# Optimization experiments

Hardware: AMD Instinct MI355X
Metric: run time of the kernel (lower is better)

## Reference

```python
import jax, jax.numpy as jnp
from jax import lax
import numpy as np

F = 257  # frequency bins; input feature dim is 2*F (mag | probability)
EPS = 1e-07


def setup_inputs() -> dict:
    key = jax.random.key(0)
    B, T = 64, 2000
    # mag (positive) and probability (in [0,1]) both drawn uniform [0,1)
    inputs = jax.random.uniform(key, (B, T, 2 * F), dtype=jnp.float32)
    # parameters, initialized as in Garch_cell.build (constants)
    Alpha = jnp.full((F,), 0.5, dtype=jnp.float32)
    beta = jnp.full((F,), 1.0, dtype=jnp.float32)
    gamma = jnp.full((F,), 0.3, dtype=jnp.float32)
    eta = jnp.full((F,), 0.6, dtype=jnp.float32)
    pi = jnp.full((F,), 1.0, dtype=jnp.float32)
    return {"inputs": inputs, "Alpha": Alpha, "beta": beta, "gamma": gamma,
            "eta": eta, "pi": pi}


def reference(inputs, Alpha, beta, gamma, eta, pi):
    # inputs: [B, T, 2F]
    mag0 = inputs[:, 0, :F]
    prob0 = inputs[:, 0, F:]
    s_init = jnp.square(mag0 * (1.0 - prob0))  # [B, F]
    carry0 = (s_init, s_init)  # (nosiy_square, ceta_e)

    x_t = jnp.swapaxes(inputs, 0, 1)  # [T, B, 2F]

    def step(carry, xt):
        s0, s1 = carry
        mag = xt[:, :F]
        p = xt[:, F:]
        mag_sq = mag * mag
        nosiy_sq = (Alpha * s0 + (1.0 - Alpha) * mag_sq) * (1.0 - p) \
                   + (beta + gamma * s1 + eta * s0) * p
        # elu(alpha=0) == relu
        clean = jax.nn.relu(mag - jnp.sqrt(nosiy_sq + EPS))
        ceta_e = jax.nn.relu(mag_sq - pi * clean * clean)
        return (nosiy_sq, ceta_e), clean

    _, outs = lax.scan(step, carry0, x_t)  # outs: [T, B, F]
    return jnp.swapaxes(outs, 0, 1)  # [B, T, F]
```

## Files before the change

### kernel.cpp

```cpp
#include <hip/hip_runtime.h>
#include <cstdint>


#define GB 64
#define GT 2000
#define GF 257
#define GEPS 1e-7f

constexpr int S2f   = 2 * GF;
constexpr int ROWB  = S2f * 4;
constexpr int OROWB = GF * 4;
constexpr int NCH   = GT / 2;
constexpr int RB    = 24;
constexpr int UNROLL = 24;

typedef float v4f  __attribute__((ext_vector_type(4)));
typedef float v4fu __attribute__((ext_vector_type(4), aligned(4)));

#define STEP(mg, pp, cv)                                                  \
  {                                                                       \
    float msq_ = (mg) * (mg);                                             \
    float u_   = fmaf(am1, msq_, a * s0);                                 \
    float v_   = fmaf(e, s0, fmaf(g, s1, be));                            \
    float ns_  = fmaf(u_, 1.0f - (pp), v_ * (pp));                        \
    float cc_  = (mg) - __builtin_amdgcn_sqrtf(ns_ + GEPS);               \
    cc_ = fmaxf(cc_, 0.0f);                                               \
    s1 = fmaxf(fmaf(-pw, cc_ * cc_, msq_), 0.0f);                         \
    s0 = ns_;                                                             \
    (cv) = cc_;                                                           \
  }

__global__ __launch_bounds__(64) void garch_kernel(
    const float* __restrict__ in,
    const float* __restrict__ Alpha,
    const float* __restrict__ beta,
    const float* __restrict__ gamma,
    const float* __restrict__ eta,
    const float* __restrict__ pi,
    float* __restrict__ out)
{
  __shared__ v4f lring[4][64];
  __shared__ __align__(16) float ob[512];
  __shared__ float td[2 * GT];

  const int lane = threadIdx.x;
  const int blk  = blockIdx.x;

  if (blk < 256) {
    const int b  = blk >> 2;
    const int f0 = (blk & 3) << 6;
    const int f  = f0 + lane;

    const float a   = Alpha[f];
    const float be  = beta[f];
    const float g   = gamma[f];
    const float e   = eta[f];
    const float pw  = pi[f];
    const float am1 = 1.0f - a;

    const uint8_t* gb = (const uint8_t*)in + (size_t)b * GT * ROWB;
    const int sub = lane >> 4;
    const int q   = lane & 15;
    const uint8_t* gsrc = gb + (size_t)(sub >> 1) * ROWB
                             + (size_t)(sub & 1) * (GF * 4)
                             + (size_t)f0 * 4 + (size_t)q * 16;

    const float* lc0 = (const float*)&lring[0][0];

    uint8_t* stp = (uint8_t*)out + (size_t)b * GT * OROWB
                 + (size_t)(lane >> 4) * OROWB
                 + (size_t)f0 * 4 + (size_t)q * 16;

    v4fu rb[RB];
    #pragma unroll
    for (int c = 2; c <= 24; ++c)
      rb[c % RB] = *(const v4fu*)(gsrc + (size_t)c * (2 * ROWB));
    {
      v4fu t0 = *(const v4fu*)(gsrc);
      v4fu t1 = *(const v4fu*)(gsrc + (size_t)(2 * ROWB));
      lring[0][lane] = t0;
      lring[1][lane] = t1;
    }

    float s0 = 0.0f, s1 = 0.0f;

    for (int sbi = 0; sbi < 1008; sbi += UNROLL) {
      #pragma unroll
      for (int u = 0; u < UNROLL; ++u) {
        const int s = sbi + u;
        if (s + 25 < NCH)
          rb[(u + 1) % RB] =
              *(const v4fu*)(gsrc + (size_t)(s + 25) * (2 * ROWB));
        __builtin_amdgcn_sched_barrier(0);
        if (s < NCH) {
          const float* lc = lc0 + (size_t)(u & 3) * 256;
          const float mg0 = lc[lane];
          const float p0  = lc[64 + lane];
          const float mg1 = lc[128 + lane];
          const float p1  = lc[192 + lane];
          if (s == 0) {
            float t = mg0 * (1.0f - p0);
            s0 = s1 = t * t;
          }
          float c0, c1;
          STEP(mg0, p0, c0);
          STEP(mg1, p1, c1);
          const int h = (u >> 1) & 1;
          ob[h * 256 + (u & 1) * 128 + lane]      = c0;
          ob[h * 256 + (u & 1) * 128 + 64 + lane] = c1;
          if ((u & 1) && s >= 3) {
            v4f od = ((const v4f*)ob)[(1 - h) * 64 + lane];
            *(v4fu*)stp = od;
            stp += 4 * OROWB;
          }
        }
        if (s + 2 < NCH)
          lring[(u + 2) & 3][lane] = rb[(u + 2) % RB];
      }
    }
    {
      v4f od = ((const v4f*)ob)[64 + lane];
      *(v4fu*)stp = od;
    }
  } else {
    const int b = blk - 256;
    const float a   = Alpha[GF - 1];
    const float be  = beta[GF - 1];
    const float g   = gamma[GF - 1];
    const float e   = eta[GF - 1];
    const float pw  = pi[GF - 1];
    const float am1 = 1.0f - a;

    const float* prow = in + (size_t)b * GT * S2f;

    float mreg[32], preg[32];
    #pragma unroll
    for (int k = 0; k < 32; ++k) {
      const int t = lane + (k << 6);
      if (t < GT) {
        mreg[k] = prow[(size_t)t * S2f + (GF - 1)];
        preg[k] = prow[(size_t)t * S2f + (2 * GF - 1)];
      }
    }
    #pragma unroll
    for (int k = 0; k < 32; ++k) {
      const int t = lane + (k << 6);
      if (t < GT) {
        td[2 * t]     = mreg[k];
        td[2 * t + 1] = preg[k];
      }
    }
    __syncthreads();

    float m0 = td[0], p0 = td[1];
    float tt = m0 * (1.0f - p0);
    float s0 = tt * tt, s1 = s0;

    for (int j = 0; j < GT / 16; ++j) {
      float mv[16], pv[16];
      #pragma unroll
      for (int r = 0; r < 16; ++r) {
        mv[r] = td[2 * (16 * j + r)];
        pv[r] = td[2 * (16 * j + r) + 1];
      }
      float creg = 0.0f;
      #pragma unroll
      for (int r = 0; r < 16; ++r) {
        float cc;
        STEP(mv[r], pv[r], cc);
        if (lane == r) creg = cc;
      }
      if (lane < 16)
        out[((size_t)(b * GT + 16 * j + lane)) * GF + (GF - 1)] = creg;
    }
  }
}

extern "C" void kernel_launch(void* const* d_in, const int* in_sizes, int n_in,
                              void* d_out, int out_size, void* d_ws, size_t ws_size,
                              hipStream_t stream) {
  const float* in    = (const float*)d_in[0];
  const float* Alpha = (const float*)d_in[1];
  const float* beta  = (const float*)d_in[2];
  const float* gamma = (const float*)d_in[3];
  const float* eta   = (const float*)d_in[4];
  const float* pi    = (const float*)d_in[5];
  float* out = (float*)d_out;

  garch_kernel<<<320, 64, 0, stream>>>(in, Alpha, beta, gamma, eta, pi, out);
}
```

Measured before the change: 482.6 us.

## Add helper wavefront that prefetches input rows into cache ahead of compute

Each block grows to two wavefronts. The second wavefront issues throwaway global loads up to a fixed number of chunks ahead of the compute wavefront, throttled by a workgroup-shared progress counter, so the compute wave's own loads hit in cache. The recurrence is latency-bound, and this targets its global-load stalls. In exchange it adds spin-polling with sleeps, extra memory traffic, and an extra wave per block competing for issue slots.

```diff
diff --git a/kernel.cpp b/kernel.cpp
--- a/kernel.cpp
+++ b/kernel.cpp
@@ -13,6 +13,7 @@
 constexpr int NCH   = GT / 2;
 constexpr int RB    = 24;
 constexpr int UNROLL = 24;
+constexpr int AHEAD = 48;
 
 typedef float v4f  __attribute__((ext_vector_type(4)));
 typedef float v4fu __attribute__((ext_vector_type(4), aligned(4)));
@@ -25,12 +26,12 @@
     float ns_  = fmaf(u_, 1.0f - (pp), v_ * (pp));                        \
     float cc_  = (mg) - __builtin_amdgcn_sqrtf(ns_ + GEPS);               \
     cc_ = fmaxf(cc_, 0.0f);                                               \
-    s1 = fmaxf(fmaf(-pw, cc_ * cc_, msq_), 0.0f);                         \
+    s1 = fmaxf(fmaf(-pw, cc_ * cc_, msq_), 0.0f);                        \
     s0 = ns_;                                                             \
     (cv) = cc_;                                                           \
   }
 
-__global__ __launch_bounds__(64) void garch_kernel(
+__global__ __launch_bounds__(128) void garch_kernel(
     const float* __restrict__ in,
     const float* __restrict__ Alpha,
     const float* __restrict__ beta,
@@ -42,21 +43,16 @@
   __shared__ v4f lring[4][64];
   __shared__ __align__(16) float ob[512];
   __shared__ float td[2 * GT];
-
-  const int lane = threadIdx.x;
+  __shared__ uint32_t prog;
+
+  const int tid  = threadIdx.x;
+  const int w    = tid >> 6;
+  const int lane = tid & 63;
   const int blk  = blockIdx.x;
 
   if (blk < 256) {
     const int b  = blk >> 2;
     const int f0 = (blk & 3) << 6;
-    const int f  = f0 + lane;
-
-    const float a   = Alpha[f];
-    const float be  = beta[f];
-    const float g   = gamma[f];
-    const float e   = eta[f];
-    const float pw  = pi[f];
-    const float am1 = 1.0f - a;
 
     const uint8_t* gb = (const uint8_t*)in + (size_t)b * GT * ROWB;
     const int sub = lane >> 4;
@@ -65,86 +61,109 @@
                              + (size_t)(sub & 1) * (GF * 4)
                              + (size_t)f0 * 4 + (size_t)q * 16;
 
-    const float* lc0 = (const float*)&lring[0][0];
-
-    uint8_t* stp = (uint8_t*)out + (size_t)b * GT * OROWB
-                 + (size_t)(lane >> 4) * OROWB
-                 + (size_t)f0 * 4 + (size_t)q * 16;
-
-    v4fu rb[RB];
-    #pragma unroll
-    for (int c = 2; c <= 24; ++c)
-      rb[c % RB] = *(const v4fu*)(gsrc + (size_t)c * (2 * ROWB));
-    {
-      v4fu t0 = *(const v4fu*)(gsrc);
-      v4fu t1 = *(const v4fu*)(gsrc + (size_t)(2 * ROWB));
-      lring[0][lane] = t0;
-      lring[1][lane] = t1;
-    }
-
-    float s0 = 0.0f, s1 = 0.0f;
-
-    for (int sbi = 0; sbi < 1008; sbi += UNROLL) {
+    if (tid == 0) prog = 0;
+    __syncthreads();
+
+    if (w == 0) {
+      const int f = f0 + lane;
+      const float a   = Alpha[f];
+      const float be  = beta[f];
+      const float g   = gamma[f];
+      const float e   = eta[f];
+      const float pw  = pi[f];
+      const float am1 = 1.0f - a;
+
+      const float* lc0 = (const float*)&lring[0][0];
+
+      uint8_t* stp = (uint8_t*)out + (size_t)b * GT * OROWB
+                   + (size_t)(lane >> 4) * OROWB
+                   + (size_t)f0 * 4 + (size_t)q * 16;
+
+      v4fu rb[RB];
       #pragma unroll
-      for (int u = 0; u < UNROLL; ++u) {
-        const int s = sbi + u;
-        if (s + 25 < NCH)
-          rb[(u + 1) % RB] =
-              *(const v4fu*)(gsrc + (size_t)(s + 25) * (2 * ROWB));
-        __builtin_amdgcn_sched_barrier(0);
-        if (s < NCH) {
-          const float* lc = lc0 + (size_t)(u & 3) * 256;
-          const float mg0 = lc[lane];
-          const float p0  = lc[64 + lane];
-          const float mg1 = lc[128 + lane];
-          const float p1  = lc[192 + lane];
-          if (s == 0) {
-            float t = mg0 * (1.0f - p0);
-            s0 = s1 = t * t;
+      for (int c = 2; c <= 24; ++c)
+        rb[c % RB] = *(const v4fu*)(gsrc + (size_t)c * (2 * ROWB));
+      {
+        v4fu t0 = *(const v4fu*)(gsrc);
+        v4fu t1 = *(const v4fu*)(gsrc + (size_t)(2 * ROWB));
+        lring[0][lane] = t0;
+        lring[1][lane] = t1;
+      }
+
+      float s0 = 0.0f, s1 = 0.0f;
+
+      for (int sbi = 0; sbi < 1008; sbi += UNROLL) {
+        #pragma unroll
+        for (int u = 0; u < UNROLL; ++u) {
+          const int s = sbi + u;
+          if (s + 25 < NCH)
+            rb[(u + 1) % RB] =
+                *(const v4fu*)(gsrc + (size_t)(s + 25) * (2 * ROWB));
+          __builtin_amdgcn_sched_barrier(0);
+          if (s < NCH) {
+            if ((u & 7) == 0 && lane == 0)
+              __hip_atomic_store(&prog, (uint32_t)s, __ATOMIC_RELAXED,
+                                 __HIP_MEMORY_SCOPE_WORKGROUP);
+            const float* lc = lc0 + (size_t)(u & 3) * 256;
+            const float mg0 = lc[lane];
+            const float p0  = lc[64 + lane];
+            const float mg1 = lc[128 + lane];
+            const float p1  = lc[192 + lane];
+            if (s == 0) {
+              float t = mg0 * (1.0f - p0);
+              s0 = s1 = t * t;
+            }
+            float c0, c1;
+            STEP(mg0, p0, c0);
+            STEP(mg1, p1, c1);
+            const int h = (u >> 1) & 1;
+            ob[h * 256 + (u & 1) * 128 + lane]      = c0;
+            ob[h * 256 + (u & 1) * 128 + 64 + lane] = c1;
+            if ((u & 1) && s >= 3) {
+              v4f od = ((const v4f*)ob)[(1 - h) * 64 + lane];
+              *(v4fu*)stp = od;
+              stp += 4 * OROWB;
+            }
           }
-          float c0, c1;
-          STEP(mg0, p0, c0);
-          STEP(mg1, p1, c1);
-          const int h = (u >> 1) & 1;
-          ob[h * 256 + (u & 1) * 128 + lane]      = c0;
-          ob[h * 256 + (u & 1) * 128 + 64 + lane] = c1;
-          if ((u & 1) && s >= 3) {
-            v4f od = ((const v4f*)ob)[(1 - h) * 64 + lane];
-            *(v4fu*)stp = od;
-            stp += 4 * OROWB;
-          }
-        }
-        if (s + 2 < NCH)
-          lring[(u + 2) & 3][lane] = rb[(u + 2) % RB];
-      }
-    }
-    {
-      v4f od = ((const v4f*)ob)[64 + lane];
-      *(v4fu*)stp = od;
+          if (s + 2 < NCH)
+            lring[(u + 2) & 3][lane] = rb[(u + 2) % RB];
+        }
+      }
+      {
+        v4f od = ((const v4f*)ob)[64 + lane];
+        *(v4fu*)stp = od;
+      }
+    } else {
+      for (int c = 24; c < NCH; ++c) {
+        while (true) {
+          uint32_t pr = __hip_atomic_load(&prog, __ATOMIC_RELAXED,
+                                          __HIP_MEMORY_SCOPE_WORKGROUP);
+          if (c - (int)pr <= AHEAD) break;
+          __builtin_amdgcn_s_sleep(2);
+        }
+        v4f dummy;
+        asm volatile("global_load_dwordx4 %0, %1, off"
+                     : "=v"(dummy)
+                     : "v"((uint64_t)(uintptr_t)(gsrc +
+                            (size_t)c * (2 * ROWB))));
+      }
     }
   } else {
     const int b = blk - 256;
-    const float a   = Alpha[GF - 1];
-    const float be  = beta[GF - 1];
-    const float g   = gamma[GF - 1];
-    const float e   = eta[GF - 1];
-    const float pw  = pi[GF - 1];
-    const float am1 = 1.0f - a;
-
     const float* prow = in + (size_t)b * GT * S2f;
 
-    float mreg[32], preg[32];
+    float mreg[16], preg[16];
     #pragma unroll
-    for (int k = 0; k < 32; ++k) {
-      const int t = lane + (k << 6);
+    for (int k = 0; k < 16; ++k) {
+      const int t = tid + (k << 7);
       if (t < GT) {
         mreg[k] = prow[(size_t)t * S2f + (GF - 1)];
         preg[k] = prow[(size_t)t * S2f + (2 * GF - 1)];
       }
     }
     #pragma unroll
-    for (int k = 0; k < 32; ++k) {
-      const int t = lane + (k << 6);
+    for (int k = 0; k < 16; ++k) {
+      const int t = tid + (k << 7);
       if (t < GT) {
         td[2 * t]     = mreg[k];
         td[2 * t + 1] = preg[k];
@@ -152,26 +171,35 @@
     }
     __syncthreads();
 
-    float m0 = td[0], p0 = td[1];
-    float tt = m0 * (1.0f - p0);
-    float s0 = tt * tt, s1 = s0;
-
-    for (int j = 0; j < GT / 16; ++j) {
-      float mv[16], pv[16];
-      #pragma unroll
-      for (int r = 0; r < 16; ++r) {
-        mv[r] = td[2 * (16 * j + r)];
-        pv[r] = td[2 * (16 * j + r) + 1];
-      }
-      float creg = 0.0f;
-      #pragma unroll
-      for (int r = 0; r < 16; ++r) {
-        float cc;
-        STEP(mv[r], pv[r], cc);
-        if (lane == r) creg = cc;
-      }
-      if (lane < 16)
-        out[((size_t)(b * GT + 16 * j + lane)) * GF + (GF - 1)] = creg;
+    if (tid < 64) {
+      const float a   = Alpha[GF - 1];
+      const float be  = beta[GF - 1];
+      const float g   = gamma[GF - 1];
+      const float e   = eta[GF - 1];
+      const float pw  = pi[GF - 1];
+      const float am1 = 1.0f - a;
+
+      float m0 = td[0], p0 = td[1];
+      float tt = m0 * (1.0f - p0);
+      float s0 = tt * tt, s1 = s0;
+
+      for (int j = 0; j < GT / 16; ++j) {
+        float mv[16], pv[16];
+        #pragma unroll
+        for (int r = 0; r < 16; ++r) {
+          mv[r] = td[2 * (16 * j + r)];
+          pv[r] = td[2 * (16 * j + r) + 1];
+        }
+        float creg = 0.0f;
+        #pragma unroll
+        for (int r = 0; r < 16; ++r) {
+          float cc;
+          STEP(mv[r], pv[r], cc);
+          if (tid == r) creg = cc;
+        }
+        if (tid < 16)
+          out[((size_t)(b * GT + 16 * j + tid)) * GF + (GF - 1)] = creg;
+      }
     }
   }
 }
@@ -187,5 +215,5 @@
   const float* pi    = (const float*)d_in[5];
   float* out = (float*)d_out;
 
-  garch_kernel<<<320, 64, 0, stream>>>(in, Alpha, beta, gamma, eta, pi, out);
+  garch_kernel<<<320, 128, 0, stream>>>(in, Alpha, beta, gamma, eta, pi, out);
 }
```

Result: no change. 483.3 us (+0.1%).
